# Kernel tuning notes

Measured on AMD Instinct MI355X. Metric: run time of the kernel, lower is better.

Reference implementation:

```python
import jax, jax.numpy as jnp
import numpy as np

B, C, L = 4, 64, 4096

def setup_inputs() -> dict:
    key = jax.random.key(0)
    ks = jax.random.split(key, 7)
    s = 1.0 / np.sqrt(C)
    return {
        "x": jax.random.normal(ks[0], (B, C, L), dtype=jnp.float32),
        "wq": jax.random.uniform(ks[1], (C, C), jnp.float32, -s, s),
        "bq": jax.random.uniform(ks[2], (C,), jnp.float32, -s, s),
        "wk": jax.random.uniform(ks[3], (C, C), jnp.float32, -s, s),
        "bk": jax.random.uniform(ks[4], (C,), jnp.float32, -s, s),
        "wv": jax.random.uniform(ks[5], (C, C), jnp.float32, -s, s),
        "bv": jax.random.uniform(ks[6], (C,), jnp.float32, -s, s),
    }

def reference(x, wq, bq, wk, bk, wv, bv):
    # x: [B, C, L]; conv1d kernel-size-1 == per-position linear over channels.
    scale = jnp.sqrt(jnp.asarray(x.shape[1], x.dtype))
    # project and move to [B, L, C]
    q = jnp.einsum('oc,bcl->blo', wq, x) + bq  # [B, L, C]
    k = jnp.einsum('oc,bcl->blo', wk, x) + bk
    v = jnp.einsum('oc,bcl->blo', wv, x) + bv
    attn = jnp.einsum('bic,bjc->bij', q, k) / scale  # [B, L, L]
    attn = jax.nn.softmax(attn, axis=-1)
    out = jnp.einsum('bij,bjc->bic', attn, v)  # [B, L, C]
    return out.transpose(0, 2, 1) + x  # back to [B, C, L] with residual
```

## Files before the change

### kernel.cpp

```cpp
#include <hip/hip_runtime.h>
#include <hip/hip_bf16.h>

typedef float    f32x4  __attribute__((ext_vector_type(4)));
typedef float    f32x16 __attribute__((ext_vector_type(16)));
typedef short    s16x4  __attribute__((ext_vector_type(4)));
typedef short    s16x8  __attribute__((ext_vector_type(8)));
typedef unsigned u32x2  __attribute__((ext_vector_type(2)));
typedef unsigned u32x4  __attribute__((ext_vector_type(4)));
typedef __bf16   bf16x8 __attribute__((ext_vector_type(8)));

#define DEVI __device__ __forceinline__

DEVI short f2bf(float f) {
    unsigned u = __builtin_bit_cast(unsigned, f);
    u += 0x8000u;
    return (short)(u >> 16);
}
DEVI float bf2f(short s) {
    return __builtin_bit_cast(float, ((unsigned)(unsigned short)s) << 16);
}
DEVI unsigned cvt_pk_bf16(float lo, float hi) {
#if defined(__HIP_DEVICE_COMPILE__)
    unsigned r;
    asm("v_cvt_pk_bf16_f32 %0, %1, %2" : "=v"(r) : "v"(lo), "v"(hi));
    return r;
#else
    return (unsigned)(unsigned short)f2bf(lo) | ((unsigned)(unsigned short)f2bf(hi) << 16);
#endif
}

DEVI float fast_exp2(float x) {
#if defined(__HIP_DEVICE_COMPILE__) && __has_builtin(__builtin_amdgcn_exp2f)
    return __builtin_amdgcn_exp2f(x);
#else
    return exp2f(x);
#endif
}

DEVI f32x4 mfma32(s16x8 a, s16x8 b, f32x4 c) {
#if defined(__HIP_DEVICE_COMPILE__) && __has_builtin(__builtin_amdgcn_mfma_f32_16x16x32_bf16)
    return __builtin_amdgcn_mfma_f32_16x16x32_bf16(
        __builtin_bit_cast(bf16x8, a), __builtin_bit_cast(bf16x8, b), c, 0, 0, 0);
#else
    asm volatile("v_mfma_f32_16x16x32_bf16 %0, %1, %2, %0" : "+v"(c) : "v"(a), "v"(b));
    return c;
#endif
}

DEVI f32x16 mfma3216(s16x8 a, s16x8 b, f32x16 c) {
#if defined(__HIP_DEVICE_COMPILE__) && __has_builtin(__builtin_amdgcn_mfma_f32_32x32x16_bf16)
    return __builtin_amdgcn_mfma_f32_32x32x16_bf16(
        __builtin_bit_cast(bf16x8, a), __builtin_bit_cast(bf16x8, b), c, 0, 0, 0);
#else
    asm volatile("v_mfma_f32_32x32x16_bf16 %0, %1, %2, %0" : "+v"(c) : "v"(a), "v"(b));
    return c;
#endif
}

DEVI void setprio1() {
#if defined(__HIP_DEVICE_COMPILE__)
    __builtin_amdgcn_s_setprio(1);
#endif
}
DEVI void setprio0() {
#if defined(__HIP_DEVICE_COMPILE__)
    __builtin_amdgcn_s_setprio(0);
#endif
}
DEVI void vm_wait4() {
#if defined(__HIP_DEVICE_COMPILE__)
    asm volatile("s_waitcnt vmcnt(4)" ::: "memory");
#endif
}
DEVI void vm_wait0() {
#if defined(__HIP_DEVICE_COMPILE__)
    asm volatile("s_waitcnt vmcnt(0)" ::: "memory");
#endif
}
DEVI void raw_barrier() {
#if defined(__HIP_DEVICE_COMPILE__)
    __builtin_amdgcn_s_barrier();
#endif
}
DEVI void sched_fence() {
#if defined(__HIP_DEVICE_COMPILE__)
    __builtin_amdgcn_sched_barrier(0);
#endif
}

DEVI void gld_lds16(const short* g, short* ldsb) {
#if defined(__HIP_DEVICE_COMPILE__) && __has_builtin(__builtin_amdgcn_global_load_lds)
    __builtin_amdgcn_global_load_lds(
        (const __attribute__((address_space(1))) void*)g,
        (__attribute__((address_space(3))) void*)ldsb, 16, 0, 0);
#endif
}

__global__ __launch_bounds__(512) void qkv_proj(
    const float* __restrict__ x,
    const float* __restrict__ wq, const float* __restrict__ bq,
    const float* __restrict__ wk, const float* __restrict__ bk,
    const float* __restrict__ wv, const float* __restrict__ bv,
    short* __restrict__ Qg, short* __restrict__ Kp, short* __restrict__ Vp)
{
    __shared__ short Xt[32 * 64];

    const int b  = blockIdx.x >> 7;
    const int l0 = (blockIdx.x & 127) * 32;
    const int t  = threadIdx.x;
    const float QS = 0.18033688011112042f;

    {
        const int c  = t & 63;
        const int lh = (t >> 6) * 4;
        const float* xr = x + ((size_t)b * 64 + c) * 4096 + l0 + lh;
        const float4 x0 = *reinterpret_cast<const float4*>(xr);
        float xv[4] = {x0.x, x0.y, x0.z, x0.w};
        #pragma unroll
        for (int i = 0; i < 4; ++i) {
            const int l = lh + i;
            Xt[l * 64 + (((c >> 3) ^ (l & 7)) * 8) + (c & 7)] = f2bf(xv[i]);
        }
    }

    const int lane = t & 63, w = t >> 6;
    const int g = lane >> 4, col = lane & 15;
    const int o0 = (w & 3) * 16;
    const int h  = w >> 2;

    s16x8 wqf[2], wkf[2], wvf[2];
    #pragma unroll
    for (int kc = 0; kc < 2; ++kc) {
        const int cb = 8 * g + 32 * kc;
        const float4 q0 = *reinterpret_cast<const float4*>(wq + (o0 + col) * 64 + cb);
        const float4 q1 = *reinterpret_cast<const float4*>(wq + (o0 + col) * 64 + cb + 4);
        const float4 k0 = *reinterpret_cast<const float4*>(wk + (o0 + col) * 64 + cb);
        const float4 k1 = *reinterpret_cast<const float4*>(wk + (o0 + col) * 64 + cb + 4);
        const float4 v0 = *reinterpret_cast<const float4*>(wv + (o0 + col) * 64 + cb);
        const float4 v1 = *reinterpret_cast<const float4*>(wv + (o0 + col) * 64 + cb + 4);
        wqf[kc][0] = f2bf(q0.x * QS); wqf[kc][1] = f2bf(q0.y * QS);
        wqf[kc][2] = f2bf(q0.z * QS); wqf[kc][3] = f2bf(q0.w * QS);
        wqf[kc][4] = f2bf(q1.x * QS); wqf[kc][5] = f2bf(q1.y * QS);
        wqf[kc][6] = f2bf(q1.z * QS); wqf[kc][7] = f2bf(q1.w * QS);
        wkf[kc][0] = f2bf(k0.x); wkf[kc][1] = f2bf(k0.y);
        wkf[kc][2] = f2bf(k0.z); wkf[kc][3] = f2bf(k0.w);
        wkf[kc][4] = f2bf(k1.x); wkf[kc][5] = f2bf(k1.y);
        wkf[kc][6] = f2bf(k1.z); wkf[kc][7] = f2bf(k1.w);
        wvf[kc][0] = f2bf(v0.x); wvf[kc][1] = f2bf(v0.y);
        wvf[kc][2] = f2bf(v0.z); wvf[kc][3] = f2bf(v0.w);
        wvf[kc][4] = f2bf(v1.x); wvf[kc][5] = f2bf(v1.y);
        wvf[kc][6] = f2bf(v1.z); wvf[kc][7] = f2bf(v1.w);
    }
    const f32x4 bq4 = *reinterpret_cast<const f32x4*>(bq + o0 + 4 * g);
    const f32x4 bk4 = *reinterpret_cast<const f32x4*>(bk + o0 + 4 * g);
    const float bvs = bv[o0 + col];

    __syncthreads();

    {
        const int row = h * 16 + col;
        const s16x8 xf0 = *reinterpret_cast<const s16x8*>(
            &Xt[row * 64 + ((g ^ (row & 7)) * 8)]);
        const s16x8 xf1 = *reinterpret_cast<const s16x8*>(
            &Xt[row * 64 + (((g + 4) ^ (row & 7)) * 8)]);

        f32x4 qa = bq4 * QS;
        qa = mfma32(wqf[0], xf0, qa);
        qa = mfma32(wqf[1], xf1, qa);
        f32x4 ka = bk4;
        ka = mfma32(wkf[0], xf0, ka);
        ka = mfma32(wkf[1], xf1, ka);
        f32x4 va = {bvs, bvs, bvs, bvs};
        va = mfma32(xf0, wvf[0], va);
        va = mfma32(xf1, wvf[1], va);

        s16x4 qs, ks;
        #pragma unroll
        for (int r = 0; r < 4; ++r) { qs[r] = f2bf(qa[r]); ks[r] = f2bf(ka[r]); }

        const int l  = l0 + row;
        const int d0 = o0 + 4 * g;
        *reinterpret_cast<s16x4*>(Qg + ((size_t)b * 4096 + l) * 64 + d0) = qs;

        {
            const int T  = l >> 6;
            const int rj = l & 63;
            const int off = rj * 64 + (((d0 >> 3) ^ (rj & 7)) << 3)
                          + ((d0 >> 2) & 1) * 4;
            *reinterpret_cast<s16x4*>(
                Kp + ((size_t)(b * 64 + T)) * 4096 + off) = ks;
        }

        {
            s16x4 vs;
            #pragma unroll
            for (int r = 0; r < 4; ++r) vs[r] = f2bf(va[r]);
            const int dV  = o0 + col;
            const int jgl = l0 + h * 16 + 4 * g;
            const int TV  = jgl >> 6;
            const int g4  = (jgl & 63) >> 2;
            const int p   = (g4 & 12) | ((g4 >> 1) & 1) | ((g4 & 1) << 1);
            const int off = dV * 64 + (((p >> 1) ^ (dV & 7)) << 3) + (p & 1) * 4;
            *reinterpret_cast<s16x4*>(
                Vp + ((size_t)(b * 64 + TV)) * 4096 + off) = vs;
        }
    }
}

__global__ __launch_bounds__(512, 2) void attn_fused(
    const short* __restrict__ Qg, const short* __restrict__ Kp,
    const short* __restrict__ Vp, const float* __restrict__ x,
    float* __restrict__ out)
{
    __shared__ short SM[49152];

    const int bid = blockIdx.x;
    const int wid = (bid & 7) * 32 + (bid >> 3);
    const int b   = wid >> 6;
    const int qt  = wid & 63;

    const int t    = threadIdx.x;
    const int w    = t >> 6;
    const int lane = t & 63;
    const int qi   = lane & 31;
    const int hi   = lane >> 5;
    const int rx   = qi & 7;
    const int s    = w & 1;
    const int h2   = (w >> 1) & 1;
    const int qs   = w >> 2;

    s16x8 qf[4];
    {
        const short* qp = Qg + ((size_t)b * 4096 + qt * 64 + qs * 32 + qi) * 64 + 8 * hi;
        qf[0] = *reinterpret_cast<const s16x8*>(qp);
        qf[1] = *reinterpret_cast<const s16x8*>(qp + 16);
        qf[2] = *reinterpret_cast<const s16x8*>(qp + 32);
        qf[3] = *reinterpret_cast<const s16x8*>(qp + 48);
    }

    const int part = w >> 1;
    const int poff = (part & 1) * 2048;
    const short* dsrc = ((part < 2) ? Kp : Vp)
        + ((size_t)(b * 64 + s * 32)) * 4096 + poff + lane * 8;
    short* dbase = SM + ((part < 2) ? 0 : 24576) + s * 3 * 4096 + poff;

    #pragma unroll
    for (int i = 0; i < 4; ++i) gld_lds16(dsrc + i * 512, dbase + i * 512);
    #pragma unroll
    for (int i = 0; i < 4; ++i)
        gld_lds16(dsrc + 4096 + i * 512, dbase + 4096 + i * 512);
    vm_wait4();
    raw_barrier();
    sched_fence();

    f32x16 oacc0 = {}, oacc1 = {};
    float lsum = 0.0f;

    const short* Kc = SM + s * 3 * 4096;
    const short* Vc = SM + 24576 + s * 3 * 4096;

    int cb = 0;
    #pragma unroll 2
    for (int tt = 0; tt < 32; ++tt) {
        if (tt < 30) {
            const int ib = (cb >= 1) ? (cb - 1) : 2;
            const short* gsrc = dsrc + (size_t)(tt + 2) * 4096;
            short* ldst = dbase + ib * 4096;
            #pragma unroll
            for (int i = 0; i < 4; ++i) gld_lds16(gsrc + i * 512, ldst + i * 512);
        }

        const short* Kl = Kc + cb * 4096;
        const short* Vl = Vc + cb * 4096;

        const short* kr = Kl + (h2 * 32 + qi) * 64;
        f32x16 S = {};
        setprio1();
        #pragma unroll
        for (int m = 0; m < 4; ++m) {
            const s16x8 a = *reinterpret_cast<const s16x8*>(
                kr + (((2 * m + hi) ^ rx) * 8));
            S = mfma3216(a, qf[m], S);
        }
        setprio0();

        const short* vr0 = Vl + qi * 64;
        const short* vr1 = Vl + (32 + qi) * 64;
        const int sA0 = ((4 * h2 + 0 + hi) ^ rx) * 8;
        const int sA1 = ((4 * h2 + 2 + hi) ^ rx) * 8;
        const s16x8 va00 = *reinterpret_cast<const s16x8*>(vr0 + sA0);
        const s16x8 va10 = *reinterpret_cast<const s16x8*>(vr1 + sA0);
        const s16x8 va01 = *reinterpret_cast<const s16x8*>(vr0 + sA1);
        const s16x8 va11 = *reinterpret_cast<const s16x8*>(vr1 + sA1);

        unsigned Pu[8];
        float ps = 0.0f;
        #pragma unroll
        for (int i = 0; i < 8; ++i) {
            const float e0 = fast_exp2(S[2 * i]);
            const float e1 = fast_exp2(S[2 * i + 1]);
            ps += e0 + e1;
            Pu[i] = cvt_pk_bf16(e0, e1);
        }
        lsum += ps;
        const u32x4 w0 = {Pu[0], Pu[1], Pu[2], Pu[3]};
        const u32x4 w1 = {Pu[4], Pu[5], Pu[6], Pu[7]};

        setprio1();
        oacc0 = mfma3216(va00, __builtin_bit_cast(s16x8, w0), oacc0);
        oacc1 = mfma3216(va10, __builtin_bit_cast(s16x8, w0), oacc1);
        oacc0 = mfma3216(va01, __builtin_bit_cast(s16x8, w1), oacc0);
        oacc1 = mfma3216(va11, __builtin_bit_cast(s16x8, w1), oacc1);
        setprio0();

        if (tt < 31) {
            if (tt < 30) vm_wait4();
            else         vm_wait0();
            raw_barrier();
            sched_fence();
        }
        cb = (cb >= 2) ? 0 : (cb + 1);
    }

    const float ltot = lsum + __shfl_xor(lsum, 32);

    __syncthreads();
    short* Po = SM;
    float* Lf = reinterpret_cast<float*>(SM + 256 * 68);
    {
        const int row = (w & 3) * 64 + qs * 32 + qi;
        #pragma unroll
        for (int db = 0; db < 2; ++db) {
            const f32x16 oa = db ? oacc1 : oacc0;
            #pragma unroll
            for (int rq = 0; rq < 4; ++rq) {
                u32x2 pk;
                pk[0] = cvt_pk_bf16(oa[4 * rq + 0], oa[4 * rq + 1]);
                pk[1] = cvt_pk_bf16(oa[4 * rq + 2], oa[4 * rq + 3]);
                const int dbase2 = 8 * rq + 4 * hi + 32 * db;
                *reinterpret_cast<u32x2*>(&Po[row * 68 + dbase2]) = pk;
            }
        }
        if (hi == 0) Lf[row] = ltot;
    }
    __syncthreads();

    {
        const int q  = t & 63;
        const int dst = (t >> 6) * 8;
        float acc[8] = {};
        float L = 0.0f;
        #pragma unroll
        for (int sh = 0; sh < 4; ++sh) {
            const int row = sh * 64 + q;
            L += Lf[row];
            const s16x4 o0 = *reinterpret_cast<const s16x4*>(&Po[row * 68 + dst]);
            const s16x4 o1 = *reinterpret_cast<const s16x4*>(&Po[row * 68 + dst + 4]);
            #pragma unroll
            for (int i = 0; i < 4; ++i) {
                acc[i]     += bf2f(o0[i]);
                acc[4 + i] += bf2f(o1[i]);
            }
        }
        const float rL = 1.0f / L;
        const size_t ob = ((size_t)b * 64 + dst) * 4096 + qt * 64 + q;
        #pragma unroll
        for (int i = 0; i < 8; ++i) {
            const size_t idx = ob + (size_t)i * 4096;
            out[idx] = fmaf(acc[i], rL, x[idx]);
        }
    }
}

extern "C" void kernel_launch(void* const* d_in, const int* in_sizes, int n_in,
                              void* d_out, int out_size, void* d_ws, size_t ws_size,
                              hipStream_t stream) {
    const float* x  = (const float*)d_in[0];
    const float* wq = (const float*)d_in[1];
    const float* bq = (const float*)d_in[2];
    const float* wk = (const float*)d_in[3];
    const float* bk = (const float*)d_in[4];
    const float* wv = (const float*)d_in[5];
    const float* bv = (const float*)d_in[6];
    float* out = (float*)d_out;

    short* Qg = reinterpret_cast<short*>(d_ws);
    short* Kp = Qg + (size_t)4 * 4096 * 64;
    short* Vp = Kp + (size_t)4 * 4096 * 64;

    qkv_proj<<<dim3(512), dim3(512), 0, stream>>>(x, wq, bq, wk, bk, wv, bv, Qg, Kp, Vp);
    attn_fused<<<dim3(256), dim3(512), 0, stream>>>(Qg, Kp, Vp, x, out);
}
```

Before: 41.01 us.

## Split attention over two key halves with a separate combine kernel

The attention kernel is split along the key dimension into two halves (split-K), doubling the grid to 512 blocks, each covering 16 key tiles with a double buffer in place of triple buffering. Each block writes partial outputs and row sums to workspace, and a new combine kernel sums the two halves, normalizes, transposes through shared memory, and adds the residual. The aim is more parallelism and occupancy on a 256-CU device, with LDS use cut so more blocks fit per CU. In exchange it adds a third launch, an extra global round trip for partials, and full __syncthreads per tile instead of the finer vmcnt waits.

Measured after the change: 42.00 us. 2.4% more time.

```diff
diff --git a/kernel.cpp b/kernel.cpp
--- a/kernel.cpp
+++ b/kernel.cpp
@@ -65,26 +65,6 @@
 DEVI void setprio0() {
 #if defined(__HIP_DEVICE_COMPILE__)
     __builtin_amdgcn_s_setprio(0);
-#endif
-}
-DEVI void vm_wait4() {
-#if defined(__HIP_DEVICE_COMPILE__)
-    asm volatile("s_waitcnt vmcnt(4)" ::: "memory");
-#endif
-}
-DEVI void vm_wait0() {
-#if defined(__HIP_DEVICE_COMPILE__)
-    asm volatile("s_waitcnt vmcnt(0)" ::: "memory");
-#endif
-}
-DEVI void raw_barrier() {
-#if defined(__HIP_DEVICE_COMPILE__)
-    __builtin_amdgcn_s_barrier();
-#endif
-}
-DEVI void sched_fence() {
-#if defined(__HIP_DEVICE_COMPILE__)
-    __builtin_amdgcn_sched_barrier(0);
 #endif
 }
 
@@ -207,16 +187,17 @@
     }
 }
 
-__global__ __launch_bounds__(512, 2) void attn_fused(
+__global__ __launch_bounds__(512, 4) void attn_part(
     const short* __restrict__ Qg, const short* __restrict__ Kp,
-    const short* __restrict__ Vp, const float* __restrict__ x,
-    float* __restrict__ out)
+    const short* __restrict__ Vp,
+    short* __restrict__ PO, float* __restrict__ PL)
 {
-    __shared__ short SM[49152];
+    __shared__ short SM[32768];
 
     const int bid = blockIdx.x;
-    const int wid = (bid & 7) * 32 + (bid >> 3);
-    const int b   = wid >> 6;
+    const int wid = (bid & 7) * 64 + (bid >> 3);
+    const int b   = wid >> 7;
+    const int sp  = (wid >> 6) & 1;
     const int qt  = wid & 63;
 
     const int t    = threadIdx.x;
@@ -241,37 +222,32 @@
     const int part = w >> 1;
     const int poff = (part & 1) * 2048;
     const short* dsrc = ((part < 2) ? Kp : Vp)
-        + ((size_t)(b * 64 + s * 32)) * 4096 + poff + lane * 8;
-    short* dbase = SM + ((part < 2) ? 0 : 24576) + s * 3 * 4096 + poff;
+        + ((size_t)(b * 64 + sp * 32 + s * 16)) * 4096 + poff + lane * 8;
+    short* dbase = SM + ((part < 2) ? 0 : 16384) + s * 2 * 4096 + poff;
 
     #pragma unroll
     for (int i = 0; i < 4; ++i) gld_lds16(dsrc + i * 512, dbase + i * 512);
-    #pragma unroll
-    for (int i = 0; i < 4; ++i)
-        gld_lds16(dsrc + 4096 + i * 512, dbase + 4096 + i * 512);
-    vm_wait4();
-    raw_barrier();
-    sched_fence();
+    __syncthreads();
 
     f32x16 oacc0 = {}, oacc1 = {};
     float lsum = 0.0f;
 
-    const short* Kc = SM + s * 3 * 4096;
-    const short* Vc = SM + 24576 + s * 3 * 4096;
-
-    int cb = 0;
+    const short* Kc = SM + s * 2 * 4096;
+    const short* Vc = SM + 16384 + s * 2 * 4096;
+
     #pragma unroll 2
-    for (int tt = 0; tt < 32; ++tt) {
-        if (tt < 30) {
-            const int ib = (cb >= 1) ? (cb - 1) : 2;
-            const short* gsrc = dsrc + (size_t)(tt + 2) * 4096;
-            short* ldst = dbase + ib * 4096;
+    for (int tt = 0; tt < 16; ++tt) {
+        const int cur = tt & 1;
+
+        if (tt < 15) {
+            const short* gsrc = dsrc + (size_t)(tt + 1) * 4096;
+            short* ldst = dbase + (cur ^ 1) * 4096;
             #pragma unroll
             for (int i = 0; i < 4; ++i) gld_lds16(gsrc + i * 512, ldst + i * 512);
         }
 
-        const short* Kl = Kc + cb * 4096;
-        const short* Vl = Vc + cb * 4096;
+        const short* Kl = Kc + cur * 4096;
+        const short* Vl = Vc + cur * 4096;
 
         const short* kr = Kl + (h2 * 32 + qi) * 64;
         f32x16 S = {};
@@ -313,18 +289,11 @@
         oacc1 = mfma3216(va11, __builtin_bit_cast(s16x8, w1), oacc1);
         setprio0();
 
-        if (tt < 31) {
-            if (tt < 30) vm_wait4();
-            else         vm_wait0();
-            raw_barrier();
-            sched_fence();
-        }
-        cb = (cb >= 2) ? 0 : (cb + 1);
+        __syncthreads();
     }
 
     const float ltot = lsum + __shfl_xor(lsum, 32);
 
-    __syncthreads();
     short* Po = SM;
     float* Lf = reinterpret_cast<float*>(SM + 256 * 68);
     {
@@ -346,28 +315,73 @@
     __syncthreads();
 
     {
-        const int q  = t & 63;
-        const int dst = (t >> 6) * 8;
+        const int q  = t >> 3;
+        const int dc = (t & 7) * 8;
         float acc[8] = {};
-        float L = 0.0f;
         #pragma unroll
         for (int sh = 0; sh < 4; ++sh) {
             const int row = sh * 64 + q;
-            L += Lf[row];
-            const s16x4 o0 = *reinterpret_cast<const s16x4*>(&Po[row * 68 + dst]);
-            const s16x4 o1 = *reinterpret_cast<const s16x4*>(&Po[row * 68 + dst + 4]);
+            const s16x4 o0 = *reinterpret_cast<const s16x4*>(&Po[row * 68 + dc]);
+            const s16x4 o1 = *reinterpret_cast<const s16x4*>(&Po[row * 68 + dc + 4]);
             #pragma unroll
             for (int i = 0; i < 4; ++i) {
                 acc[i]     += bf2f(o0[i]);
                 acc[4 + i] += bf2f(o1[i]);
             }
         }
+        u32x4 pk;
+        pk[0] = cvt_pk_bf16(acc[0], acc[1]);
+        pk[1] = cvt_pk_bf16(acc[2], acc[3]);
+        pk[2] = cvt_pk_bf16(acc[4], acc[5]);
+        pk[3] = cvt_pk_bf16(acc[6], acc[7]);
+        *reinterpret_cast<u32x4*>(
+            PO + ((size_t)(sp * 4 + b) * 4096 + qt * 64 + q) * 64 + dc) = pk;
+        if (t < 64) {
+            PL[(size_t)(sp * 4 + b) * 4096 + qt * 64 + t] =
+                Lf[t] + Lf[64 + t] + Lf[128 + t] + Lf[192 + t];
+        }
+    }
+}
+
+__global__ __launch_bounds__(256) void attn_combine(
+    const short* __restrict__ PO, const float* __restrict__ PL,
+    const float* __restrict__ x, float* __restrict__ out)
+{
+    __shared__ float T[64][34];
+
+    const int b  = blockIdx.x >> 7;
+    const int q0 = (blockIdx.x & 127) * 32;
+    const int t  = threadIdx.x;
+
+    {
+        const int ql = t >> 3;
+        const int dc = (t & 7) * 8;
+        const int q  = q0 + ql;
+
+        const size_t r0 = (size_t)(0 + b) * 4096 + q;
+        const size_t r1 = (size_t)(4 + b) * 4096 + q;
+        const float L = PL[r0] + PL[r1];
+        const s16x8 o0 = *reinterpret_cast<const s16x8*>(PO + r0 * 64 + dc);
+        const s16x8 o1 = *reinterpret_cast<const s16x8*>(PO + r1 * 64 + dc);
         const float rL = 1.0f / L;
-        const size_t ob = ((size_t)b * 64 + dst) * 4096 + qt * 64 + q;
-        #pragma unroll
-        for (int i = 0; i < 8; ++i) {
-            const size_t idx = ob + (size_t)i * 4096;
-            out[idx] = fmaf(acc[i], rL, x[idx]);
+        #pragma unroll
+        for (int i = 0; i < 8; ++i)
+            T[dc + i][ql] = (bf2f(o0[i]) + bf2f(o1[i])) * rL;
+    }
+    __syncthreads();
+    {
+        const int d  = t >> 2;
+        const int qc = (t & 3) * 8;
+        const size_t ob = ((size_t)b * 64 + d) * 4096 + q0 + qc;
+        #pragma unroll
+        for (int i = 0; i < 8; i += 4) {
+            const float4 xv = *reinterpret_cast<const float4*>(x + ob + i);
+            float4 o4;
+            o4.x = T[d][qc + i + 0] + xv.x;
+            o4.y = T[d][qc + i + 1] + xv.y;
+            o4.z = T[d][qc + i + 2] + xv.z;
+            o4.w = T[d][qc + i + 3] + xv.w;
+            *reinterpret_cast<float4*>(out + ob + i) = o4;
         }
     }
 }
@@ -387,7 +401,10 @@
     short* Qg = reinterpret_cast<short*>(d_ws);
     short* Kp = Qg + (size_t)4 * 4096 * 64;
     short* Vp = Kp + (size_t)4 * 4096 * 64;
+    short* PO = Vp + (size_t)4 * 4096 * 64;
+    float* PL = reinterpret_cast<float*>(PO + (size_t)8 * 4096 * 64);
 
     qkv_proj<<<dim3(512), dim3(512), 0, stream>>>(x, wq, bq, wk, bk, wv, bv, Qg, Kp, Vp);
-    attn_fused<<<dim3(256), dim3(512), 0, stream>>>(Qg, Kp, Vp, x, out);
-}
+    attn_part<<<dim3(512), dim3(512), 0, stream>>>(Qg, Kp, Vp, PO, PL);
+    attn_combine<<<dim3(512), dim3(256), 0, stream>>>(PO, PL, x, out);
+}
```
